# Optimization experiments

Measured on AMD Instinct MI355X. Metric: run time of the kernel, lower is better.

## Reference

```python
import jax, jax.numpy as jnp
import numpy as np
import math

D_MODEL = 1024
N_HEAD = 16


def _layer_norm(x, w, b, eps=1e-5):
    mu = jnp.mean(x, axis=-1, keepdims=True)
    var = jnp.var(x, axis=-1, keepdims=True)
    return (x - mu) * jax.lax.rsqrt(var + eps) * w + b


def setup_inputs() -> dict:
    key = jax.random.key(0)
    ks = jax.random.split(key, 8)
    d = D_MODEL
    s = 0.02
    return {
        "x": jax.random.normal(ks[0], (2, 2048, d), dtype=jnp.float32),
        "ln1_w": jnp.ones((d,), jnp.float32),
        "ln1_b": jnp.zeros((d,), jnp.float32),
        "qkv_w": jax.random.normal(ks[1], (d, 3 * d), jnp.float32) * s,
        "qkv_b": jnp.zeros((3 * d,), jnp.float32),
        "attn_out_w": jax.random.normal(ks[2], (d, d), jnp.float32) * s,
        "attn_out_b": jnp.zeros((d,), jnp.float32),
        "ln2_w": jnp.ones((d,), jnp.float32),
        "ln2_b": jnp.zeros((d,), jnp.float32),
        "c_fc_w": jax.random.normal(ks[3], (d, 4 * d), jnp.float32) * s,
        "c_fc_b": jnp.zeros((4 * d,), jnp.float32),
        "c_proj_w": jax.random.normal(ks[4], (4 * d, d), jnp.float32) * s,
        "c_proj_b": jnp.zeros((d,), jnp.float32),
    }


def _block(x, ln1_w, ln1_b, qkv_w, qkv_b, attn_out_w, attn_out_b,
           ln2_w, ln2_b, c_fc_w, c_fc_b, c_proj_w, c_proj_b):
    B, S, D = x.shape
    H = N_HEAD
    hd = D // H

    # pre-LN (NOTE: original code overwrites x with ln_1(x), so the
    # attention residual is around the *normalized* input)
    xn = _layer_norm(x, ln1_w, ln1_b)

    qkv = xn @ qkv_w + qkv_b                       # [B,S,3D]
    q, k, v = jnp.split(qkv, 3, axis=-1)
    q = q.reshape(B, S, H, hd).transpose(0, 2, 1, 3)  # [B,H,S,hd]
    k = k.reshape(B, S, H, hd).transpose(0, 2, 1, 3)
    v = v.reshape(B, S, H, hd).transpose(0, 2, 1, 3)

    scale = 1.0 / math.sqrt(hd)
    scores = jnp.einsum("bhqd,bhkd->bhqk", q, k) * scale
    causal = jnp.tril(jnp.ones((S, S), dtype=bool))
    scores = jnp.where(causal, scores, -jnp.inf)
    attn = jax.nn.softmax(scores, axis=-1)
    o = jnp.einsum("bhqk,bhkd->bhqd", attn, v)
    o = o.transpose(0, 2, 1, 3).reshape(B, S, D)
    o = o @ attn_out_w + attn_out_b                # attention output

    h = xn + o                                     # residual around ln_1 output
    hn = _layer_norm(h, ln2_w, ln2_b)
    mlp = jax.nn.gelu(hn @ c_fc_w + c_fc_b, approximate=False) @ c_proj_w + c_proj_b
    return hn + mlp                                # residual around ln_2 output


def reference(x, ln1_w, ln1_b, qkv_w, qkv_b, attn_out_w, attn_out_b,
              ln2_w, ln2_b, c_fc_w, c_fc_b, c_proj_w, c_proj_b):
    return _block(x, ln1_w, ln1_b, qkv_w, qkv_b, attn_out_w, attn_out_b,
                  ln2_w, ln2_b, c_fc_w, c_fc_b, c_proj_w, c_proj_b)
```

## Files before the change

### kernel.cpp

```cpp
#include <hip/hip_runtime.h>
#include <math.h>

#define D_MODEL 1024
#define SEQ     2048
#define BATCH   2
#define NHEAD   16
#define ROWS    (BATCH*SEQ)

typedef __attribute__((ext_vector_type(8))) short  bf16x8;
typedef __attribute__((ext_vector_type(4))) float  f32x4;

__device__ __forceinline__ float bf2f(short u) {
    union { unsigned int i; float f; } x;
    x.i = ((unsigned int)(unsigned short)u) << 16;
    return x.f;
}
__device__ __forceinline__ short f2bf(float f) {
    unsigned int u = __float_as_uint(f);
    unsigned int r = (u + 0x7FFFu + ((u >> 16) & 1u)) >> 16;
    return (short)r;
}
__device__ __forceinline__ unsigned int packbf2(float a, float b) {
    return (unsigned int)(unsigned short)f2bf(a)
         | ((unsigned int)(unsigned short)f2bf(b) << 16);
}
__device__ __forceinline__ void gload_lds16(const void* g, void* l) {
    __builtin_amdgcn_global_load_lds(
        (const __attribute__((address_space(1))) unsigned int*)g,
        (__attribute__((address_space(3))) unsigned int*)l, 16, 0, 0);
}
__device__ __forceinline__ float wave_sum(float v) {
#pragma unroll
    for (int o = 32; o > 0; o >>= 1) v += __shfl_xor(v, o, 64);
    return v;
}

__global__ __launch_bounds__(256) void ln_kernel(
    const float* __restrict__ in, const float* __restrict__ w,
    const float* __restrict__ b, float* __restrict__ outF,
    short* __restrict__ outB)
{
    const int row = blockIdx.x;
    const int tid = threadIdx.x;
    const float4 v = ((const float4*)(in + (size_t)row * D_MODEL))[tid];
    float s  = v.x + v.y + v.z + v.w;
    float ss = v.x*v.x + v.y*v.y + v.z*v.z + v.w*v.w;
    s  = wave_sum(s);
    ss = wave_sum(ss);
    __shared__ float red[2][4];
    const int wid = tid >> 6, lane = tid & 63;
    if (lane == 0) { red[0][wid] = s; red[1][wid] = ss; }
    __syncthreads();
    const float ts  = red[0][0] + red[0][1] + red[0][2] + red[0][3];
    const float tss = red[1][0] + red[1][1] + red[1][2] + red[1][3];
    const float mean = ts * (1.0f / D_MODEL);
    const float var  = tss * (1.0f / D_MODEL) - mean * mean;
    const float inv  = rsqrtf(var + 1e-5f);
    const float4 wv = ((const float4*)w)[tid];
    const float4 bv = ((const float4*)b)[tid];
    float o0 = (v.x - mean) * inv * wv.x + bv.x;
    float o1 = (v.y - mean) * inv * wv.y + bv.y;
    float o2 = (v.z - mean) * inv * wv.z + bv.z;
    float o3 = (v.w - mean) * inv * wv.w + bv.w;
    if (outF) {
        float4 o = make_float4(o0, o1, o2, o3);
        ((float4*)(outF + (size_t)row * D_MODEL))[tid] = o;
    }
    ushort4 ob;
    ob.x = (unsigned short)f2bf(o0); ob.y = (unsigned short)f2bf(o1);
    ob.z = (unsigned short)f2bf(o2); ob.w = (unsigned short)f2bf(o3);
    ((ushort4*)(outB + (size_t)row * D_MODEL))[tid] = ob;
}

__global__ __launch_bounds__(256) void wprep(
    const float* __restrict__ W, short* __restrict__ Wt, int K, int N)
{
    __shared__ float t[32][33];
    const int kk = blockIdx.y << 5, nn = blockIdx.x << 5;
    const int r = threadIdx.x >> 3, c = (threadIdx.x & 7) << 2;
    const float4 v = *(const float4*)(W + (size_t)(kk + r) * N + nn + c);
    t[r][c + 0] = v.x; t[r][c + 1] = v.y; t[r][c + 2] = v.z; t[r][c + 3] = v.w;
    __syncthreads();
    ushort4 o;
    o.x = (unsigned short)f2bf(t[c + 0][r]);
    o.y = (unsigned short)f2bf(t[c + 1][r]);
    o.z = (unsigned short)f2bf(t[c + 2][r]);
    o.w = (unsigned short)f2bf(t[c + 3][r]);
    *(ushort4*)(Wt + (size_t)(nn + r) * K + kk + c) = o;
}

template<bool GELU>
__global__ __launch_bounds__(256) void gemm_mfma(
    const short* __restrict__ A, const short* __restrict__ Bt,
    const float* __restrict__ bias, const float* __restrict__ res,
    float* __restrict__ outF, short* __restrict__ outB,
    int M, int N, int K, int lda)
{
    __shared__ short smem[32768];
    const int tid = threadIdx.x;
    const int wid = tid >> 6, lane = tid & 63;
    const int wm = wid >> 1, wn = wid & 1;
    const int m0 = blockIdx.y << 7, n0 = blockIdx.x << 7;

    const int srow = lane >> 3;
    const int gseg = ((lane & 7) ^ srow) << 3;
    const short* Ag = A  + (size_t)(m0 + (wid << 5) + srow) * lda + gseg;
    const short* Bg = Bt + (size_t)(n0 + (wid << 5) + srow) * lda + gseg;

#define STAGE(buf, k0) do { \
        const int lb = ((buf) << 14) + (wid << 11); \
        _Pragma("unroll") \
        for (int j = 0; j < 4; ++j) { \
            gload_lds16(Ag + (k0) + (size_t)(j << 3) * lda, \
                        &smem[lb + (j << 9)]); \
            gload_lds16(Bg + (k0) + (size_t)(j << 3) * lda, \
                        &smem[lb + 8192 + (j << 9)]); \
        } \
    } while (0)

    f32x4 acc[4][4];
#pragma unroll
    for (int i = 0; i < 4; ++i)
#pragma unroll
        for (int j = 0; j < 4; ++j) acc[i][j] = (f32x4){0.f, 0.f, 0.f, 0.f};

    const int frow = lane & 15;
    const int g = lane >> 4;
    const int xs0 = ((g)     ^ (frow & 7)) << 3;
    const int xs1 = ((g + 4) ^ (frow & 7)) << 3;

    const int niter = K >> 6;
    STAGE(0, 0);
    __syncthreads();
    int cur = 0;
    for (int it = 0; it < niter; ++it) {
        if (it + 1 < niter) STAGE(cur ^ 1, (it + 1) << 6);

        const int ab = (cur << 14);
        const int bb = (cur << 14) + 8192;
#pragma unroll
        for (int kh = 0; kh < 2; ++kh) {
            const int xs = kh ? xs1 : xs0;
            bf16x8 af[4], bfv[4];
#pragma unroll
            for (int mt = 0; mt < 4; ++mt)
                af[mt] = *(const bf16x8*)
                    &smem[ab + (((wm << 6) + (mt << 4) + frow) << 6) + xs];
#pragma unroll
            for (int nt = 0; nt < 4; ++nt)
                bfv[nt] = *(const bf16x8*)
                    &smem[bb + (((wn << 6) + (nt << 4) + frow) << 6) + xs];
#pragma unroll
            for (int mt = 0; mt < 4; ++mt)
#pragma unroll
                for (int nt = 0; nt < 4; ++nt)
                    acc[mt][nt] = __builtin_amdgcn_mfma_f32_16x16x32_bf16(
                        af[mt], bfv[nt], acc[mt][nt], 0, 0, 0);
        }
        __syncthreads();
        cur ^= 1;
    }
#undef STAGE

    const int lrow = g << 2;
    const int lcol = frow;

    if (outB) {
#pragma unroll
        for (int nt = 0; nt < 4; ++nt) {
            const int cl = (wn << 6) + (nt << 4) + lcol;
            const float bv = bias[n0 + cl];
#pragma unroll
            for (int mt = 0; mt < 4; ++mt)
#pragma unroll
                for (int r = 0; r < 4; ++r) {
                    const int rl = (wm << 6) + (mt << 4) + lrow + r;
                    float v = acc[mt][nt][r] + bv;
                    if (GELU) v = 0.5f * v * (1.0f + erff(v * 0.70710678118654752f));
                    smem[(rl << 7) + (cl ^ (((rl >> 2) & 3) << 4))] = f2bf(v);
                }
        }
        __syncthreads();
        const int row = tid >> 1, c0 = (tid & 1) << 6;
        const int sw = ((row >> 2) & 3) << 4;
        short* gp = outB + (size_t)(m0 + row) * N + n0 + c0;
#pragma unroll
        for (int j = 0; j < 8; ++j)
            *(uint4*)(gp + (j << 3)) =
                *(const uint4*)&smem[(row << 7) + ((c0 + (j << 3)) ^ sw)];
        return;
    }

#pragma unroll
    for (int nt = 0; nt < 4; ++nt) {
        const int col = n0 + (wn << 6) + (nt << 4) + lcol;
        const float bv = bias[col];
#pragma unroll
        for (int mt = 0; mt < 4; ++mt) {
#pragma unroll
            for (int r = 0; r < 4; ++r) {
                const int row = m0 + (wm << 6) + (mt << 4) + lrow + r;
                float v = acc[mt][nt][r] + bv;
                if (GELU) v = 0.5f * v * (1.0f + erff(v * 0.70710678118654752f));
                if (res)  v += res[(size_t)row * N + col];
                outF[(size_t)row * N + col] = v;
            }
        }
    }
}

__global__ __launch_bounds__(256) void attn3(
    const short* __restrict__ qkv,
    short* __restrict__ o)
{
    int wg = blockIdx.x;
    wg = (wg & 7) * 128 + (wg >> 3);
    const int qb = wg & 31;
    const int bh = wg >> 5;
    const int b = bh >> 4, h = bh & 15;
    const int tid = threadIdx.x;
    const int w = tid >> 6, lane = tid & 63;
    const int g = lane >> 4, fr = lane & 15;
    const int qbase = qb << 6;

    __shared__ short Ks[64 * 64];
    __shared__ short Vt[64 * 72];
    __shared__ short Ps[4 * 16 * 72];

    const size_t qrow = (size_t)(b * SEQ + qbase + (w << 4) + fr);
    const short* qp = qkv + qrow * 3072 + h * 64 + (g << 3);
    const bf16x8 qf0 = *(const bf16x8*)qp;
    const bf16x8 qf1 = *(const bf16x8*)(qp + 32);

    f32x4 oT[4];
#pragma unroll
    for (int i = 0; i < 4; ++i) oT[i] = (f32x4){0.f, 0.f, 0.f, 0.f};
    float lsum = 0.f;

    const int krow = lane >> 3, kseg = lane & 7;
    const int kpair = tid & 31, vd0 = (tid >> 5) << 3;
    short* PsW = &Ps[(w << 4) * 72];
    const int qloc = (w << 4) + fr;

    for (int t = 0; t <= qb; ++t) {
        const int k0 = t << 6;
        __syncthreads();
        {
            const int key0 = (w << 4) + krow;
            const int sw = (kseg ^ krow) << 3;
            const short* kgp = qkv + (size_t)(b * SEQ + k0 + key0) * 3072
                               + 1024 + h * 64 + sw;
            gload_lds16(kgp,                 &Ks[((w << 4) + 0) << 6]);
            gload_lds16(kgp + (size_t)8 * 3072, &Ks[((w << 4) + 8) << 6]);
        }
        {
            const short* vp = qkv + (size_t)(b * SEQ + k0 + (kpair << 1)) * 3072
                              + 2048 + h * 64 + vd0;
            const bf16x8 va = *(const bf16x8*)vp;
            const bf16x8 vb = *(const bf16x8*)(vp + 3072);
#pragma unroll
            for (int i = 0; i < 8; ++i)
                *(unsigned int*)&Vt[(vd0 + i) * 72 + (kpair << 1)] =
                    (unsigned int)(unsigned short)va[i]
                    | ((unsigned int)(unsigned short)vb[i] << 16);
        }
        __syncthreads();

        f32x4 sT[4];
#pragma unroll
        for (int i = 0; i < 4; ++i) sT[i] = (f32x4){0.f, 0.f, 0.f, 0.f};
#pragma unroll
        for (int kh = 0; kh < 2; ++kh) {
            const bf16x8 qf = kh ? qf1 : qf0;
            const int tseg = g + (kh << 2);
#pragma unroll
            for (int mt = 0; mt < 4; ++mt) {
                const int key = (mt << 4) + fr;
                const bf16x8 kf = *(const bf16x8*)
                    &Ks[(key << 6) + ((tseg ^ (key & 7)) << 3)];
                sT[mt] = __builtin_amdgcn_mfma_f32_16x16x32_bf16(
                    kf, qf, sT[mt], 0, 0, 0);
            }
        }

        const bool diag = (t == qb);
#pragma unroll
        for (int mt = 0; mt < 4; ++mt) {
            float p0 = __expf(0.125f * sT[mt][0]);
            float p1 = __expf(0.125f * sT[mt][1]);
            float p2 = __expf(0.125f * sT[mt][2]);
            float p3 = __expf(0.125f * sT[mt][3]);
            if (diag) {
                const int key = (mt << 4) + (g << 2);
                if (key + 0 > qloc) p0 = 0.f;
                if (key + 1 > qloc) p1 = 0.f;
                if (key + 2 > qloc) p2 = 0.f;
                if (key + 3 > qloc) p3 = 0.f;
            }
            lsum += (p0 + p1) + (p2 + p3);
            *(uint2*)&PsW[fr * 72 + (mt << 4) + (g << 2)] =
                make_uint2(packbf2(p0, p1), packbf2(p2, p3));
        }

#pragma unroll
        for (int kh = 0; kh < 2; ++kh) {
            const bf16x8 pf = *(const bf16x8*)
                &PsW[fr * 72 + (g << 3) + (kh << 5)];
#pragma unroll
            for (int mt = 0; mt < 4; ++mt) {
                const bf16x8 vf = *(const bf16x8*)
                    &Vt[((mt << 4) + fr) * 72 + (g << 3) + (kh << 5)];
                oT[mt] = __builtin_amdgcn_mfma_f32_16x16x32_bf16(
                    vf, pf, oT[mt], 0, 0, 0);
            }
        }
    }

    lsum += __shfl_xor(lsum, 16, 64);
    lsum += __shfl_xor(lsum, 32, 64);
    const float rl = 1.0f / lsum;
    short* orow = o + qrow * D_MODEL + h * 64;
#pragma unroll
    for (int mt = 0; mt < 4; ++mt) {
        *(uint2*)&orow[(mt << 4) + (g << 2)] = make_uint2(
            packbf2(oT[mt][0] * rl, oT[mt][1] * rl),
            packbf2(oT[mt][2] * rl, oT[mt][3] * rl));
    }
}

extern "C" void kernel_launch(void* const* d_in, const int* in_sizes, int n_in,
                              void* d_out, int out_size, void* d_ws, size_t ws_size,
                              hipStream_t stream) {
    const float* x          = (const float*)d_in[0];
    const float* ln1_w      = (const float*)d_in[1];
    const float* ln1_b      = (const float*)d_in[2];
    const float* qkv_w      = (const float*)d_in[3];
    const float* qkv_b      = (const float*)d_in[4];
    const float* attn_out_w = (const float*)d_in[5];
    const float* attn_out_b = (const float*)d_in[6];
    const float* ln2_w      = (const float*)d_in[7];
    const float* ln2_b      = (const float*)d_in[8];
    const float* c_fc_w     = (const float*)d_in[9];
    const float* c_fc_b     = (const float*)d_in[10];
    const float* c_proj_w   = (const float*)d_in[11];
    const float* c_proj_b   = (const float*)d_in[12];
    float* out = (float*)d_out;

    char* W = (char*)d_ws;
    float* xn_f   = (float*)W;
    char*  poolA  = W + 16777216;
    short* xn_b   = (short*)poolA;
    short* qkvbuf = (short*)(poolA + 8388608);
    short* attn_b = (short*)poolA;
    short* fc_b   = (short*)poolA;
    short* hn_b   = (short*)(poolA + 33554432);
    short* wts    = (short*)(poolA + 33554432 + 8388608);
    short* qkvw_t = wts;
    short* attnw_t= wts + 3145728;
    short* fcw_t  = wts + 4194304;
    short* projw_t= wts + 8388608;

    const dim3 blk(256);

    wprep<<<dim3(3072/32, 1024/32), blk, 0, stream>>>(qkv_w, qkvw_t, 1024, 3072);
    wprep<<<dim3(1024/32, 1024/32), blk, 0, stream>>>(attn_out_w, attnw_t, 1024, 1024);
    wprep<<<dim3(4096/32, 1024/32), blk, 0, stream>>>(c_fc_w, fcw_t, 1024, 4096);
    wprep<<<dim3(1024/32, 4096/32), blk, 0, stream>>>(c_proj_w, projw_t, 4096, 1024);

    ln_kernel<<<ROWS, blk, 0, stream>>>(x, ln1_w, ln1_b, xn_f, xn_b);
    gemm_mfma<false><<<dim3(24, 32), blk, 0, stream>>>(
        xn_b, qkvw_t, qkv_b, nullptr, nullptr, qkvbuf, ROWS, 3072, 1024, 1024);
    attn3<<<dim3(32 * 32), blk, 0, stream>>>(qkvbuf, attn_b);
    gemm_mfma<false><<<dim3(8, 32), blk, 0, stream>>>(
        attn_b, attnw_t, attn_out_b, xn_f, xn_f, nullptr, ROWS, 1024, 1024, 1024);
    ln_kernel<<<ROWS, blk, 0, stream>>>(xn_f, ln2_w, ln2_b, out, hn_b);
    gemm_mfma<true><<<dim3(32, 32), blk, 0, stream>>>(
        hn_b, fcw_t, c_fc_b, nullptr, nullptr, fc_b, ROWS, 4096, 1024, 1024);
    gemm_mfma<false><<<dim3(8, 32), blk, 0, stream>>>(
        fc_b, projw_t, c_proj_b, out, out, nullptr, ROWS, 1024, 4096, 4096);
}
```

Baseline: 395.7 us.

## Deepen GEMM prefetch, pair causal attention blocks, use hardware bf16 pack

The GEMM main loop now prefetches two stages ahead. It replaces __syncthreads with explicit vmcnt waits and raw s_barrier, so global loads overlap more MFMA work. The attention kernel now pairs query block i with block 31-i in each workgroup, which balances the causal work per block and halves the grid. It also raises wave priority around the MFMA sections. Float-to-bf16 packing switches from software rounding to the v_cvt_pk_bf16_f32 instruction. The hand-written waitcnt count and barrier placement risk races if the STAGE load count differs from the assumed 8 outstanding loads.

```diff
diff --git a/kernel.cpp b/kernel.cpp
--- a/kernel.cpp
+++ b/kernel.cpp
@@ -20,9 +20,10 @@
     unsigned int r = (u + 0x7FFFu + ((u >> 16) & 1u)) >> 16;
     return (short)r;
 }
-__device__ __forceinline__ unsigned int packbf2(float a, float b) {
-    return (unsigned int)(unsigned short)f2bf(a)
-         | ((unsigned int)(unsigned short)f2bf(b) << 16);
+__device__ __forceinline__ unsigned int cvt_pk_bf16(float lo, float hi) {
+    unsigned int r;
+    asm("v_cvt_pk_bf16_f32 %0, %1, %2" : "=v"(r) : "v"(lo), "v"(hi));
+    return r;
 }
 __device__ __forceinline__ void gload_lds16(const void* g, void* l) {
     __builtin_amdgcn_global_load_lds(
@@ -66,10 +67,8 @@
         float4 o = make_float4(o0, o1, o2, o3);
         ((float4*)(outF + (size_t)row * D_MODEL))[tid] = o;
     }
-    ushort4 ob;
-    ob.x = (unsigned short)f2bf(o0); ob.y = (unsigned short)f2bf(o1);
-    ob.z = (unsigned short)f2bf(o2); ob.w = (unsigned short)f2bf(o3);
-    ((ushort4*)(outB + (size_t)row * D_MODEL))[tid] = ob;
+    uint2 ob = make_uint2(cvt_pk_bf16(o0, o1), cvt_pk_bf16(o2, o3));
+    ((uint2*)(outB + (size_t)row * D_MODEL))[tid] = ob;
 }
 
 __global__ __launch_bounds__(256) void wprep(
@@ -131,10 +130,12 @@
 
     const int niter = K >> 6;
     STAGE(0, 0);
-    __syncthreads();
+    if (niter > 1) STAGE(1, 64);
     int cur = 0;
     for (int it = 0; it < niter; ++it) {
-        if (it + 1 < niter) STAGE(cur ^ 1, (it + 1) << 6);
+        if (it + 1 < niter) asm volatile("s_waitcnt vmcnt(8)" ::: "memory");
+        else                asm volatile("s_waitcnt vmcnt(0)" ::: "memory");
+        asm volatile("s_barrier" ::: "memory");
 
         const int ab = (cur << 14);
         const int bb = (cur << 14) + 8192;
@@ -157,7 +158,8 @@
                     acc[mt][nt] = __builtin_amdgcn_mfma_f32_16x16x32_bf16(
                         af[mt], bfv[nt], acc[mt][nt], 0, 0, 0);
         }
-        __syncthreads();
+        asm volatile("s_barrier" ::: "memory");
+        if (it + 2 < niter) STAGE(cur, (it + 2) << 6);
         cur ^= 1;
     }
 #undef STAGE
@@ -214,117 +216,127 @@
     short* __restrict__ o)
 {
     int wg = blockIdx.x;
-    wg = (wg & 7) * 128 + (wg >> 3);
-    const int qb = wg & 31;
-    const int bh = wg >> 5;
+    wg = (wg & 7) * 64 + (wg >> 3);
+    const int pair = wg & 15;
+    const int bh = wg >> 4;
     const int b = bh >> 4, h = bh & 15;
     const int tid = threadIdx.x;
     const int w = tid >> 6, lane = tid & 63;
     const int g = lane >> 4, fr = lane & 15;
-    const int qbase = qb << 6;
 
     __shared__ short Ks[64 * 64];
     __shared__ short Vt[64 * 72];
     __shared__ short Ps[4 * 16 * 72];
-
-    const size_t qrow = (size_t)(b * SEQ + qbase + (w << 4) + fr);
-    const short* qp = qkv + qrow * 3072 + h * 64 + (g << 3);
-    const bf16x8 qf0 = *(const bf16x8*)qp;
-    const bf16x8 qf1 = *(const bf16x8*)(qp + 32);
-
-    f32x4 oT[4];
-#pragma unroll
-    for (int i = 0; i < 4; ++i) oT[i] = (f32x4){0.f, 0.f, 0.f, 0.f};
-    float lsum = 0.f;
 
     const int krow = lane >> 3, kseg = lane & 7;
     const int kpair = tid & 31, vd0 = (tid >> 5) << 3;
     short* PsW = &Ps[(w << 4) * 72];
     const int qloc = (w << 4) + fr;
 
-    for (int t = 0; t <= qb; ++t) {
-        const int k0 = t << 6;
+#pragma unroll
+    for (int ph = 0; ph < 2; ++ph) {
+        const int qb = ph ? (31 - pair) : pair;
+        const int qbase = qb << 6;
+
+        const size_t qrow = (size_t)(b * SEQ + qbase + (w << 4) + fr);
+        const short* qp = qkv + qrow * 3072 + h * 64 + (g << 3);
+        const bf16x8 qf0 = *(const bf16x8*)qp;
+        const bf16x8 qf1 = *(const bf16x8*)(qp + 32);
+
+        f32x4 oT[4];
+#pragma unroll
+        for (int i = 0; i < 4; ++i) oT[i] = (f32x4){0.f, 0.f, 0.f, 0.f};
+        float lsum = 0.f;
+
+        for (int t = 0; t <= qb; ++t) {
+            const int k0 = t << 6;
+            __syncthreads();
+            {
+                const int key0 = (w << 4) + krow;
+                const int sw = (kseg ^ krow) << 3;
+                const short* kgp = qkv + (size_t)(b * SEQ + k0 + key0) * 3072
+                                   + 1024 + h * 64 + sw;
+                gload_lds16(kgp,                    &Ks[((w << 4) + 0) << 6]);
+                gload_lds16(kgp + (size_t)8 * 3072, &Ks[((w << 4) + 8) << 6]);
+            }
+            {
+                const short* vp = qkv + (size_t)(b * SEQ + k0 + (kpair << 1)) * 3072
+                                  + 2048 + h * 64 + vd0;
+                const bf16x8 va = *(const bf16x8*)vp;
+                const bf16x8 vb = *(const bf16x8*)(vp + 3072);
+#pragma unroll
+                for (int i = 0; i < 8; ++i)
+                    *(unsigned int*)&Vt[(vd0 + i) * 72 + (kpair << 1)] =
+                        (unsigned int)(unsigned short)va[i]
+                        | ((unsigned int)(unsigned short)vb[i] << 16);
+            }
+            __syncthreads();
+
+            f32x4 sT[4];
+#pragma unroll
+            for (int i = 0; i < 4; ++i) sT[i] = (f32x4){0.f, 0.f, 0.f, 0.f};
+            __builtin_amdgcn_s_setprio(1);
+#pragma unroll
+            for (int kh = 0; kh < 2; ++kh) {
+                const bf16x8 qf = kh ? qf1 : qf0;
+                const int tseg = g + (kh << 2);
+#pragma unroll
+                for (int mt = 0; mt < 4; ++mt) {
+                    const int key = (mt << 4) + fr;
+                    const bf16x8 kf = *(const bf16x8*)
+                        &Ks[(key << 6) + ((tseg ^ (key & 7)) << 3)];
+                    sT[mt] = __builtin_amdgcn_mfma_f32_16x16x32_bf16(
+                        kf, qf, sT[mt], 0, 0, 0);
+                }
+            }
+            __builtin_amdgcn_s_setprio(0);
+
+            const bool diag = (t == qb);
+#pragma unroll
+            for (int mt = 0; mt < 4; ++mt) {
+                float p0 = __expf(0.125f * sT[mt][0]);
+                float p1 = __expf(0.125f * sT[mt][1]);
+                float p2 = __expf(0.125f * sT[mt][2]);
+                float p3 = __expf(0.125f * sT[mt][3]);
+                if (diag) {
+                    const int key = (mt << 4) + (g << 2);
+                    if (key + 0 > qloc) p0 = 0.f;
+                    if (key + 1 > qloc) p1 = 0.f;
+                    if (key + 2 > qloc) p2 = 0.f;
+                    if (key + 3 > qloc) p3 = 0.f;
+                }
+                lsum += (p0 + p1) + (p2 + p3);
+                *(uint2*)&PsW[fr * 72 + (mt << 4) + (g << 2)] =
+                    make_uint2(cvt_pk_bf16(p0, p1), cvt_pk_bf16(p2, p3));
+            }
+
+            __builtin_amdgcn_s_setprio(1);
+#pragma unroll
+            for (int kh = 0; kh < 2; ++kh) {
+                const bf16x8 pf = *(const bf16x8*)
+                    &PsW[fr * 72 + (g << 3) + (kh << 5)];
+#pragma unroll
+                for (int mt = 0; mt < 4; ++mt) {
+                    const bf16x8 vf = *(const bf16x8*)
+                        &Vt[((mt << 4) + fr) * 72 + (g << 3) + (kh << 5)];
+                    oT[mt] = __builtin_amdgcn_mfma_f32_16x16x32_bf16(
+                        vf, pf, oT[mt], 0, 0, 0);
+                }
+            }
+            __builtin_amdgcn_s_setprio(0);
+        }
+
+        lsum += __shfl_xor(lsum, 16, 64);
+        lsum += __shfl_xor(lsum, 32, 64);
+        const float rl = 1.0f / lsum;
+        short* orow = o + qrow * D_MODEL + h * 64;
+#pragma unroll
+        for (int mt = 0; mt < 4; ++mt) {
+            *(uint2*)&orow[(mt << 4) + (g << 2)] = make_uint2(
+                cvt_pk_bf16(oT[mt][0] * rl, oT[mt][1] * rl),
+                cvt_pk_bf16(oT[mt][2] * rl, oT[mt][3] * rl));
+        }
         __syncthreads();
-        {
-            const int key0 = (w << 4) + krow;
-            const int sw = (kseg ^ krow) << 3;
-            const short* kgp = qkv + (size_t)(b * SEQ + k0 + key0) * 3072
-                               + 1024 + h * 64 + sw;
-            gload_lds16(kgp,                 &Ks[((w << 4) + 0) << 6]);
-            gload_lds16(kgp + (size_t)8 * 3072, &Ks[((w << 4) + 8) << 6]);
-        }
-        {
-            const short* vp = qkv + (size_t)(b * SEQ + k0 + (kpair << 1)) * 3072
-                              + 2048 + h * 64 + vd0;
-            const bf16x8 va = *(const bf16x8*)vp;
-            const bf16x8 vb = *(const bf16x8*)(vp + 3072);
-#pragma unroll
-            for (int i = 0; i < 8; ++i)
-                *(unsigned int*)&Vt[(vd0 + i) * 72 + (kpair << 1)] =
-                    (unsigned int)(unsigned short)va[i]
-                    | ((unsigned int)(unsigned short)vb[i] << 16);
-        }
-        __syncthreads();
-
-        f32x4 sT[4];
-#pragma unroll
-        for (int i = 0; i < 4; ++i) sT[i] = (f32x4){0.f, 0.f, 0.f, 0.f};
-#pragma unroll
-        for (int kh = 0; kh < 2; ++kh) {
-            const bf16x8 qf = kh ? qf1 : qf0;
-            const int tseg = g + (kh << 2);
-#pragma unroll
-            for (int mt = 0; mt < 4; ++mt) {
-                const int key = (mt << 4) + fr;
-                const bf16x8 kf = *(const bf16x8*)
-                    &Ks[(key << 6) + ((tseg ^ (key & 7)) << 3)];
-                sT[mt] = __builtin_amdgcn_mfma_f32_16x16x32_bf16(
-                    kf, qf, sT[mt], 0, 0, 0);
-            }
-        }
-
-        const bool diag = (t == qb);
-#pragma unroll
-        for (int mt = 0; mt < 4; ++mt) {
-            float p0 = __expf(0.125f * sT[mt][0]);
-            float p1 = __expf(0.125f * sT[mt][1]);
-            float p2 = __expf(0.125f * sT[mt][2]);
-            float p3 = __expf(0.125f * sT[mt][3]);
-            if (diag) {
-                const int key = (mt << 4) + (g << 2);
-                if (key + 0 > qloc) p0 = 0.f;
-                if (key + 1 > qloc) p1 = 0.f;
-                if (key + 2 > qloc) p2 = 0.f;
-                if (key + 3 > qloc) p3 = 0.f;
-            }
-            lsum += (p0 + p1) + (p2 + p3);
-            *(uint2*)&PsW[fr * 72 + (mt << 4) + (g << 2)] =
-                make_uint2(packbf2(p0, p1), packbf2(p2, p3));
-        }
-
-#pragma unroll
-        for (int kh = 0; kh < 2; ++kh) {
-            const bf16x8 pf = *(const bf16x8*)
-                &PsW[fr * 72 + (g << 3) + (kh << 5)];
-#pragma unroll
-            for (int mt = 0; mt < 4; ++mt) {
-                const bf16x8 vf = *(const bf16x8*)
-                    &Vt[((mt << 4) + fr) * 72 + (g << 3) + (kh << 5)];
-                oT[mt] = __builtin_amdgcn_mfma_f32_16x16x32_bf16(
-                    vf, pf, oT[mt], 0, 0, 0);
-            }
-        }
-    }
-
-    lsum += __shfl_xor(lsum, 16, 64);
-    lsum += __shfl_xor(lsum, 32, 64);
-    const float rl = 1.0f / lsum;
-    short* orow = o + qrow * D_MODEL + h * 64;
-#pragma unroll
-    for (int mt = 0; mt < 4; ++mt) {
-        *(uint2*)&orow[(mt << 4) + (g << 2)] = make_uint2(
-            packbf2(oT[mt][0] * rl, oT[mt][1] * rl),
-            packbf2(oT[mt][2] * rl, oT[mt][3] * rl));
     }
 }
 
@@ -370,7 +382,7 @@
     ln_kernel<<<ROWS, blk, 0, stream>>>(x, ln1_w, ln1_b, xn_f, xn_b);
     gemm_mfma<false><<<dim3(24, 32), blk, 0, stream>>>(
         xn_b, qkvw_t, qkv_b, nullptr, nullptr, qkvbuf, ROWS, 3072, 1024, 1024);
-    attn3<<<dim3(32 * 32), blk, 0, stream>>>(qkvbuf, attn_b);
+    attn3<<<dim3(512), blk, 0, stream>>>(qkvbuf, attn_b);
     gemm_mfma<false><<<dim3(8, 32), blk, 0, stream>>>(
         attn_b, attnw_t, attn_out_b, xn_f, xn_f, nullptr, ROWS, 1024, 1024, 1024);
     ln_kernel<<<ROWS, blk, 0, stream>>>(xn_f, ln2_w, ln2_b, out, hn_b);
```

New measurement: 367.1 us. 1.08x faster.
